# Optimization experiments

Measured on AMD Instinct MI355X. Metric: run time of the kernel, lower is better.

The kernel has to match this reference:

```python
import jax, jax.numpy as jnp
import numpy as np

N = 100000   # nodes per graph
E = 1200000  # edges per graph
D_IN = 64
FILTERS = [128, 128, 64]
K_SLICES = 16
MLP = [32, 16, 8, 4]


def setup_inputs() -> dict:
    key = jax.random.key(0)
    ks = jax.random.split(key, 24)
    s = 0.1
    inp = {
        'x_i': jax.random.normal(ks[0], (N, D_IN), jnp.float32),
        'edge_index_i': jax.random.randint(ks[1], (2, E), 0, N, jnp.int64),
        'x_j': jax.random.normal(ks[2], (N, D_IN), jnp.float32),
        'edge_index_j': jax.random.randint(ks[3], (2, E), 0, N, jnp.int64),
    }
    # GCN conv stack params: 64->128->128->64
    dims = [D_IN] + FILTERS
    for li in range(3):
        inp[f'conv_w{li}'] = jax.random.normal(ks[4 + 2 * li], (dims[li], dims[li + 1]), jnp.float32) * s
        inp[f'conv_b{li}'] = jnp.zeros((dims[li + 1],), jnp.float32)
    d = FILTERS[-1]
    inp['att_w'] = jax.random.normal(ks[10], (d, d), jnp.float32) * s
    inp['ntn_wt'] = jax.random.normal(ks[11], (K_SLICES, d, d), jnp.float32) * s
    inp['ntn_wm'] = jax.random.normal(ks[12], (K_SLICES, 2 * d), jnp.float32) * s
    inp['ntn_b'] = jnp.zeros((K_SLICES,), jnp.float32)
    mdims = [K_SLICES] + MLP
    for li in range(4):
        inp[f'mlp_w{li}'] = jax.random.normal(ks[13 + 2 * li], (mdims[li], mdims[li + 1]), jnp.float32) * s
        inp[f'mlp_b{li}'] = jnp.zeros((mdims[li + 1],), jnp.float32)
    inp['score_w'] = jax.random.normal(ks[22], (MLP[-1], 1), jnp.float32) * s
    inp['score_b'] = jnp.zeros((1,), jnp.float32)
    return inp


def _gcn(x, W, b, src, dst):
    # PyG GCNConv: add self loops, symmetric normalization, aggregate into dst.
    n = x.shape[0]
    loop = jnp.arange(n, dtype=src.dtype)
    src = jnp.concatenate([src, loop])
    dst = jnp.concatenate([dst, loop])
    deg = jax.ops.segment_sum(jnp.ones_like(dst, dtype=x.dtype), dst, num_segments=n)
    dinv = jax.lax.rsqrt(deg)  # deg >= 1 due to self loops
    norm = dinv[src] * dinv[dst]             # [E+N]
    xw = x @ W                               # [N, Dout]
    out = jax.ops.segment_sum(xw[src] * norm[:, None], dst, num_segments=n)
    return out + b


def _attention(x, Wa):
    # global context attention pooling over nodes
    gc = jnp.tanh(jnp.mean(x @ Wa, axis=0))          # [D]
    att = jax.nn.sigmoid(x @ gc)                     # [N]
    return jnp.sum(x * att[:, None], axis=0)         # [D]


def _ntn(h_i, h_j, Wt, Wm, b):
    # s_k = h_i^T Wt[k] h_j + Wm[k] . [h_i; h_j] + b_k, then tanh
    bilinear = jnp.einsum('d,kde,e->k', h_i, Wt, h_j)
    linear = Wm @ jnp.concatenate([h_i, h_j])
    return jnp.tanh(bilinear + linear + b)           # [K]


def reference(x_i, edge_index_i, x_j, edge_index_j,
              conv_w0, conv_b0, conv_w1, conv_b1, conv_w2, conv_b2,
              att_w, ntn_wt, ntn_wm, ntn_b,
              mlp_w0, mlp_b0, mlp_w1, mlp_b1, mlp_w2, mlp_b2, mlp_w3, mlp_b3,
              score_w, score_b):
    convs = [(conv_w0, conv_b0), (conv_w1, conv_b1), (conv_w2, conv_b2)]
    si, di = edge_index_i[0], edge_index_i[1]
    sj, dj = edge_index_j[0], edge_index_j[1]
    for li, (W, b) in enumerate(convs):
        x_i = _gcn(x_i, W, b, si, di)
        x_j = _gcn(x_j, W, b, sj, dj)
        if li < len(convs) - 1:
            x_i = jax.nn.relu(x_i)
            x_j = jax.nn.relu(x_j)
    h_i = _attention(x_i, att_w)
    h_j = _attention(x_j, att_w)
    z = _ntn(h_i, h_j, ntn_wt, ntn_wm, ntn_b)        # [K]
    for W, b in [(mlp_w0, mlp_b0), (mlp_w1, mlp_b1), (mlp_w2, mlp_b2), (mlp_w3, mlp_b3)]:
        z = jax.nn.relu(z @ W + b)
    return z @ score_w + score_b                     # [1]
```

## Files before the change

### kernel.cpp

```cpp
#include <hip/hip_runtime.h>
#include <cstdint>
#include <cstddef>

#define CDIV(a,b) (((a)+(b)-1)/(b))

typedef __attribute__((ext_vector_type(8))) unsigned short ushort8v;
typedef __attribute__((ext_vector_type(8))) short short8v;
typedef __attribute__((ext_vector_type(4))) float f32x4;
typedef __attribute__((ext_vector_type(2))) float f32x2;

constexpr int BCAP = 8192;
constexpr int CPAD = 256 * BCAP;

__device__ __forceinline__ float bf2f(unsigned short u) {
  return __uint_as_float(((unsigned)u) << 16);
}
__device__ __forceinline__ unsigned short f2bf(float f) {
  unsigned u = __float_as_uint(f);
  unsigned r = (u + 0x7fff + ((u >> 16) & 1)) >> 16;
  return (unsigned short)r;
}

__device__ __forceinline__ void acc_fp8(float* acc, uint2 v) {
  f32x2 p;
  p = __builtin_amdgcn_cvt_pk_f32_fp8((int)v.x, false); acc[0] += p[0]; acc[1] += p[1];
  p = __builtin_amdgcn_cvt_pk_f32_fp8((int)v.x, true);  acc[2] += p[0]; acc[3] += p[1];
  p = __builtin_amdgcn_cvt_pk_f32_fp8((int)v.y, false); acc[4] += p[0]; acc[5] += p[1];
  p = __builtin_amdgcn_cvt_pk_f32_fp8((int)v.y, true);  acc[6] += p[0]; acc[7] += p[1];
}


__global__ void k_prep(const float* __restrict__ w0, const float* __restrict__ w1,
                       const float* __restrict__ w2,
                       unsigned short* __restrict__ w0p, unsigned short* __restrict__ w1p,
                       unsigned short* __restrict__ w2p,
                       int* __restrict__ gcur, double* __restrict__ gcsum,
                       double* __restrict__ hsum) {
  int id = blockIdx.x * 256 + threadIdx.x;
  if (id < 512) gcur[id] = 0;
  else if (id < 640) gcsum[id - 512] = 0.0;
  else if (id < 768) hsum[id - 640] = 0.0;
  if (id < 8192) {
    int k = id / 128, n = id % 128;
    w0p[n * 64 + ((((k >> 3) + n) & 7) * 8) + (k & 7)] = f2bf(w0[id]);
  }
  if (id < 16384) {
    int k = id / 128, n = id % 128;
    w1p[n * 128 + ((((k >> 3) + n) & 15) * 8) + (k & 7)] = f2bf(w1[id]);
  }
  if (id < 8192) {
    int k = id / 64, n = id % 64;
    w2p[n * 128 + ((((k >> 3) + n) & 15) * 8) + (k & 7)] = f2bf(w2[id]);
  }
}


__global__ __launch_bounds__(256) void k_place(const int* __restrict__ src0,
                                               const int* __restrict__ dst0,
                                               const int* __restrict__ src1,
                                               const int* __restrict__ dst1,
                                               int E, int N,
                                               int* __restrict__ gcur,
                                               unsigned* __restrict__ part) {
  __shared__ int bcnt[256], bbase[256], bcur[256];
  int g = blockIdx.y;
  const int* src = g ? src1 : src0;
  const int* dst = g ? dst1 : dst0;
  int t = threadIdx.x;
  int e0 = blockIdx.x * 4096, e1 = min(e0 + 4096, E);
  bcnt[t] = 0;
  __syncthreads();
  for (int e = e0 + t; e < e1; e += 256) atomicAdd(&bcnt[dst[e] >> 9], 1);
  __syncthreads();
  bbase[t] = t * BCAP + (bcnt[t] ? atomicAdd(&gcur[g * 256 + t], bcnt[t]) : 0);
  bcur[t] = 0;
  __syncthreads();
  unsigned* pg = part + (size_t)g * CPAD;
  for (int e = e0 + t; e < e1; e += 256) {
    int d = dst[e], s = src[e];
    int b = d >> 9;
    int off = atomicAdd(&bcur[b], 1);
    pg[bbase[b] + off] = ((unsigned)(d & 511) << 18) | (unsigned)(s + g * N);
  }
}


__global__ __launch_bounds__(256) void k_build(const unsigned* __restrict__ part,
                                               const int* __restrict__ gcur,
                                               int2* __restrict__ rowp2, int* __restrict__ col,
                                               float* __restrict__ dinv, int n) {
  __shared__ int cnt[512], off[512], tmp[256];
  int g = blockIdx.y, b = blockIdx.x;
  int lo = b << 9;
  if (lo >= n) return;
  int t = threadIdx.x;
  int s0 = b * BCAP;
  int cntE = gcur[g * 256 + b];
  const unsigned* pg = part + (size_t)g * CPAD;
  cnt[t] = 0; cnt[t + 256] = 0;
  __syncthreads();
  for (int e = s0 + t; e < s0 + cntE; e += 256) atomicAdd(&cnt[pg[e] >> 18], 1);
  __syncthreads();
  int a0 = cnt[2 * t], a1 = cnt[2 * t + 1];
  int ps = a0 + a1;
  tmp[t] = ps; __syncthreads();
  for (int o = 1; o < 256; o <<= 1) {
    int x = (t >= o) ? tmp[t - o] : 0;
    __syncthreads();
    tmp[t] += x;
    __syncthreads();
  }
  int ex = tmp[t] - ps;
  off[2 * t] = ex;
  off[2 * t + 1] = ex + a0;
  __syncthreads();
  for (int i = t; i < 512; i += 256) {
    int node = lo + i;
    if (node < n) {
      int st = g * CPAD + s0 + off[i];
      rowp2[g * n + node] = make_int2(st, st + cnt[i]);
      dinv[g * n + node] = rsqrtf((float)(cnt[i] + 1));
    }
  }
  __syncthreads();
  for (int e = s0 + t; e < s0 + cntE; e += 256) {
    unsigned pr = pg[e];
    int p = atomicAdd(&off[pr >> 18], 1);
    col[g * CPAD + s0 + p] = (int)(pr & 0x3FFFFu);
  }
}


__global__ void k_tofp8(const float* __restrict__ in0, const float* __restrict__ in1,
                        const float* __restrict__ dinv,
                        uint2* __restrict__ out, int n8half, int n8) {
  int i = blockIdx.x * blockDim.x + threadIdx.x;
  if (i < n8) {
    const float4* i4 = (i < n8half) ? (const float4*)in0 : (const float4*)in1;
    int ii = (i < n8half) ? i : i - n8half;
    float di = dinv[i >> 3];
    float4 a = i4[2 * ii], b = i4[2 * ii + 1];
    int lo = __builtin_amdgcn_cvt_pk_fp8_f32(di * a.x, di * a.y, 0, false);
    lo = __builtin_amdgcn_cvt_pk_fp8_f32(di * a.z, di * a.w, lo, true);
    int hi = __builtin_amdgcn_cvt_pk_fp8_f32(di * b.x, di * b.y, 0, false);
    hi = __builtin_amdgcn_cvt_pk_fp8_f32(di * b.z, di * b.w, hi, true);
    out[i] = make_uint2((unsigned)lo, (unsigned)hi);
  }
}


template<int D, bool ADD_BIAS, bool COLSUM>
__device__ __forceinline__ void agg_body(
    const unsigned char* __restrict__ xin, unsigned short* __restrict__ xout,
    const int2* __restrict__ rowp2, const int* __restrict__ col,
    const float* __restrict__ dinv, const float* __restrict__ bias, int n,
    float* __restrict__ partial) {
  constexpr int G = D / 8;
  constexpr int NPB = 256 / G;
  int node = blockIdx.x * NPB + threadIdx.x / G;
  int g = threadIdx.x % G;
  const uint2* x8 = (const uint2*)xin;
  float r[8];
  if (node < n) {
    float di = dinv[node];
    float acc[8];
#pragma unroll
    for (int j = 0; j < 8; ++j) acc[j] = 0.f;
    acc_fp8(acc, x8[(size_t)node * G + g]);
    int2 rp = rowp2[node];
    int e = rp.x, e1 = rp.y;
    for (; e + 4 <= e1; e += 4) {
      int s0 = col[e], s1 = col[e + 1], s2 = col[e + 2], s3 = col[e + 3];
      uint2 v0 = x8[(size_t)s0 * G + g];
      uint2 v1 = x8[(size_t)s1 * G + g];
      uint2 v2 = x8[(size_t)s2 * G + g];
      uint2 v3 = x8[(size_t)s3 * G + g];
      acc_fp8(acc, v0); acc_fp8(acc, v1);
      acc_fp8(acc, v2); acc_fp8(acc, v3);
    }
    for (; e < e1; ++e) {
      int s = col[e];
      acc_fp8(acc, x8[(size_t)s * G + g]);
    }
#pragma unroll
    for (int j = 0; j < 8; ++j) {
      r[j] = di * acc[j];
      if (ADD_BIAS) r[j] += bias[g * 8 + j];
    }
    ushort8v o;
#pragma unroll
    for (int j = 0; j < 8; ++j) o[j] = f2bf(r[j]);
    ((ushort8v*)xout)[(size_t)node * G + g] = o;
  } else {
#pragma unroll
    for (int j = 0; j < 8; ++j) r[j] = 0.f;
  }
  if (COLSUM) {
    __shared__ float ws[4][64];
    int lane = threadIdx.x & 63, wave = threadIdx.x >> 6;
#pragma unroll
    for (int j = 0; j < 8; ++j) {
      float v = r[j];
      v += __shfl_xor(v, 8);
      v += __shfl_xor(v, 16);
      v += __shfl_xor(v, 32);
      r[j] = v;
    }
    if (lane < 8) {
#pragma unroll
      for (int j = 0; j < 8; ++j) ws[wave][lane * 8 + j] = r[j];
    }
    __syncthreads();
    int t = threadIdx.x;
    if (t < 64) partial[(size_t)blockIdx.x * 64 + t] = ws[0][t] + ws[1][t] + ws[2][t] + ws[3][t];
  }
}

__global__ __launch_bounds__(256) void k_aggL0(
    const unsigned char* __restrict__ x, unsigned short* __restrict__ o,
    const int2* __restrict__ rp, const int* __restrict__ col,
    const float* __restrict__ dv, int n) {
  agg_body<64, false, false>(x, o, rp, col, dv, nullptr, n, nullptr);
}
__global__ __launch_bounds__(256) void k_aggL1(
    const unsigned char* __restrict__ x, unsigned short* __restrict__ o,
    const int2* __restrict__ rp, const int* __restrict__ col,
    const float* __restrict__ dv, int n) {
  agg_body<128, false, false>(x, o, rp, col, dv, nullptr, n, nullptr);
}
__global__ __launch_bounds__(256) void k_aggF(
    const unsigned char* __restrict__ x, unsigned short* __restrict__ o,
    const int2* __restrict__ rp, const int* __restrict__ col,
    const float* __restrict__ dv, const float* __restrict__ bias, int n,
    float* __restrict__ partial) {
  agg_body<64, true, true>(x, o, rp, col, dv, bias, n, partial);
}


template<int K, int DOUT, bool RELU, bool PRESCALE, bool OUTFP8>
__device__ __forceinline__ void gemm_body(
    const unsigned short* __restrict__ A, const unsigned short* __restrict__ Wp,
    const float* __restrict__ bias, void* __restrict__ Cv,
    const float* __restrict__ dinv, int n) {
  constexpr int CPR = K / 8;
  constexpr int CM = CPR - 1;
  constexpr int NT = DOUT / 16;
  __shared__ unsigned short As[128 * K];
  __shared__ unsigned short Ws[DOUT * K];
  int t = threadIdx.x;
  int blockM = blockIdx.x * 128;

#pragma unroll
  for (int id = t; id < 128 * CPR; id += 256) {
    int r = id / CPR, c = id % CPR;
    int grow = blockM + r;
    ushort8v v = {0, 0, 0, 0, 0, 0, 0, 0};
    if (grow < n) v = ((const ushort8v*)A)[(size_t)grow * CPR + c];
    *(ushort8v*)&As[r * K + ((c + r) & CM) * 8] = v;
  }
#pragma unroll
  for (int id = t; id < DOUT * CPR; id += 256)
    ((ushort8v*)Ws)[id] = ((const ushort8v*)Wp)[id];
  __syncthreads();

  int lane = t & 63, wave = t >> 6;
  int m15 = lane & 15, quad = lane >> 4;
  f32x4 acc[2][NT];
#pragma unroll
  for (int i = 0; i < 2; ++i)
#pragma unroll
    for (int j = 0; j < NT; ++j) acc[i][j] = (f32x4){0.f, 0.f, 0.f, 0.f};

  int i0 = wave * 32 + m15;
  int i1 = i0 + 16;
#pragma unroll
  for (int kc = 0; kc < K; kc += 32) {
    int c0 = (kc >> 3) + quad;
    short8v a0 = *(const short8v*)&As[i0 * K + ((c0 + i0) & CM) * 8];
    short8v a1 = *(const short8v*)&As[i1 * K + ((c0 + i1) & CM) * 8];
    short8v b[NT];
#pragma unroll
    for (int nt = 0; nt < NT; ++nt) {
      int nn = nt * 16 + m15;
      b[nt] = *(const short8v*)&Ws[nn * K + ((c0 + nn) & CM) * 8];
    }
#pragma unroll
    for (int nt = 0; nt < NT; ++nt) {
      acc[0][nt] = __builtin_amdgcn_mfma_f32_16x16x32_bf16(a0, b[nt], acc[0][nt], 0, 0, 0);
      acc[1][nt] = __builtin_amdgcn_mfma_f32_16x16x32_bf16(a1, b[nt], acc[1][nt], 0, 0, 0);
    }
  }

#pragma unroll
  for (int rt = 0; rt < 2; ++rt) {
    int rbase = blockM + wave * 32 + rt * 16 + quad * 4;
#pragma unroll
    for (int nt = 0; nt < NT; ++nt) {
      int colg = nt * 16 + m15;
      float bv = bias ? bias[colg] : 0.f;
#pragma unroll
      for (int r = 0; r < 4; ++r) {
        int row = rbase + r;
        if (row < n) {
          float v = acc[rt][nt][r] + bv;
          if (RELU) v = fmaxf(v, 0.f);
          if (PRESCALE) v *= dinv[row];
          if (OUTFP8) {
            int b8 = __builtin_amdgcn_cvt_pk_fp8_f32(v, v, 0, false);
            ((unsigned char*)Cv)[(size_t)row * DOUT + colg] = (unsigned char)(b8 & 0xff);
          } else {
            ((unsigned short*)Cv)[(size_t)row * DOUT + colg] = f2bf(v);
          }
        }
      }
    }
  }
}

__global__ __launch_bounds__(256) void k_gemmL0(
    const unsigned short* __restrict__ A, const unsigned short* __restrict__ Wp,
    const float* __restrict__ bias, void* __restrict__ C,
    const float* __restrict__ dv, int n) {
  gemm_body<64, 128, true, true, true>(A, Wp, bias, C, dv, n);
}
__global__ __launch_bounds__(256) void k_gemmL1(
    const unsigned short* __restrict__ A, const unsigned short* __restrict__ Wp,
    const float* __restrict__ bias, void* __restrict__ C,
    const float* __restrict__ dv, int n) {
  gemm_body<128, 128, true, false, false>(A, Wp, bias, C, dv, n);
}
__global__ __launch_bounds__(256) void k_gemmL2(
    const unsigned short* __restrict__ A, const unsigned short* __restrict__ Wp,
    const float* __restrict__ bias, void* __restrict__ C,
    const float* __restrict__ dv, int n) {
  gemm_body<128, 64, false, true, true>(A, Wp, bias, C, dv, n);
}


__global__ __launch_bounds__(256) void k_cm2(const float* __restrict__ partial, int nbg,
                                             double* __restrict__ gcsum) {
  __shared__ double sd[256];
  int g = blockIdx.y, t = threadIdx.x;
  int f = t & 63, rg = t >> 6;
  double acc = 0.0;
  for (int b = blockIdx.x * 4 + rg; b < nbg; b += gridDim.x * 4)
    acc += (double)partial[(size_t)(g * nbg + b) * 64 + f];
  sd[t] = acc; __syncthreads();
  if (t < 64) {
    double tot = sd[t] + sd[t + 64] + sd[t + 128] + sd[t + 192];
    atomicAdd(&gcsum[g * 64 + t], tot);
  }
}


__global__ void k_hsum(const unsigned short* __restrict__ x, const double* __restrict__ gcsum,
                       const float* __restrict__ Wa, int N, int n2,
                       double* __restrict__ hsum) {
  __shared__ float m[128], gcs[128];
  __shared__ double sd[256][4];
  int t = threadIdx.x;
  if (t < 128) m[t] = (float)(gcsum[t] / (double)N);
  __syncthreads();
  if (t < 128) {
    int gg = t >> 6, f = t & 63;
    float s = 0.f;
    for (int d = 0; d < 64; ++d) s += m[gg * 64 + d] * Wa[d * 64 + f];
    gcs[t] = tanhf(s);
  }
  __syncthreads();
  int g = t & 15, sub = t >> 4;
  float4 gcv0 = ((const float4*)gcs)[g];
  float4 gcv1 = ((const float4*)gcs)[16 + g];
  double a[2][4];
#pragma unroll
  for (int j = 0; j < 4; ++j) { a[0][j] = 0.0; a[1][j] = 0.0; }
  for (int node = blockIdx.x * 16 + sub; node < n2; node += gridDim.x * 16) {
    int gid = node >= N;
    float4 gcv = gid ? gcv1 : gcv0;
    ushort4 xu = ((const ushort4*)x)[(size_t)node * 16 + g];
    float x0 = bf2f(xu.x), x1 = bf2f(xu.y), x2 = bf2f(xu.z), x3 = bf2f(xu.w);
    float p = x0 * gcv.x + x1 * gcv.y + x2 * gcv.z + x3 * gcv.w;
    p += __shfl_xor(p, 1);
    p += __shfl_xor(p, 2);
    p += __shfl_xor(p, 4);
    p += __shfl_xor(p, 8);
    float att = 1.f / (1.f + expf(-p));
    a[gid][0] += (double)(att * x0); a[gid][1] += (double)(att * x1);
    a[gid][2] += (double)(att * x2); a[gid][3] += (double)(att * x3);
  }
#pragma unroll 1
  for (int gid = 0; gid < 2; ++gid) {
    sd[t][0] = a[gid][0]; sd[t][1] = a[gid][1];
    sd[t][2] = a[gid][2]; sd[t][3] = a[gid][3];
    __syncthreads();
    if (t < 64) {
      int gg = t >> 2, j = t & 3;
      double tot = 0;
      for (int w = 0; w < 16; ++w) tot += sd[w * 16 + gg][j];
      if (tot != 0.0) atomicAdd(&hsum[gid * 64 + t], tot);
    }
    __syncthreads();
  }
}


__global__ __launch_bounds__(1024) void k_final(
    const double* __restrict__ hsum,
    const float* __restrict__ Wt, const float* __restrict__ Wm,
    const float* __restrict__ bn,
    const float* __restrict__ w0, const float* __restrict__ b0,
    const float* __restrict__ w1, const float* __restrict__ b1,
    const float* __restrict__ w2, const float* __restrict__ b2,
    const float* __restrict__ w3, const float* __restrict__ b3,
    const float* __restrict__ sw, const float* __restrict__ sb,
    float* __restrict__ out) {
  __shared__ float hi[64], hj[64], red[1024], z[16], u[32], v[16], w[8], q[4];
  int t = threadIdx.x;
  if (t < 64) hi[t] = (float)hsum[t];
  else if (t < 128) hj[t - 64] = (float)hsum[t];
  __syncthreads();
  int k = t >> 6, r = t & 63;
  const float* wr = Wt + ((size_t)k * 64 + r) * 64;
  float s = 0.f;
#pragma unroll 8
  for (int c = 0; c < 64; ++c) s += wr[c] * hj[c];
  float p = hi[r] * s;
  p += Wm[k * 128 + r] * hi[r] + Wm[k * 128 + 64 + r] * hj[r];
  red[t] = p;
  __syncthreads();
  for (int o = 32; o > 0; o >>= 1) {
    if (r < o) red[t] += red[t + o];
    __syncthreads();
  }
  if (t < 16) z[t] = tanhf(red[t * 64] + bn[t]);
  __syncthreads();
  if (t < 32) {
    float ss = b0[t];
    for (int i = 0; i < 16; ++i) ss += z[i] * w0[i * 32 + t];
    u[t] = fmaxf(ss, 0.f);
  }
  __syncthreads();
  if (t < 16) {
    float ss = b1[t];
    for (int i = 0; i < 32; ++i) ss += u[i] * w1[i * 16 + t];
    v[t] = fmaxf(ss, 0.f);
  }
  __syncthreads();
  if (t < 8) {
    float ss = b2[t];
    for (int i = 0; i < 16; ++i) ss += v[i] * w2[i * 8 + t];
    w[t] = fmaxf(ss, 0.f);
  }
  __syncthreads();
  if (t < 4) {
    float ss = b3[t];
    for (int i = 0; i < 8; ++i) ss += w[i] * w3[i * 4 + t];
    q[t] = fmaxf(ss, 0.f);
  }
  __syncthreads();
  if (t == 0) {
    float ss = sb[0];
    for (int i = 0; i < 4; ++i) ss += q[i] * sw[i];
    out[0] = ss;
  }
}


extern "C" void kernel_launch(void* const* d_in, const int* in_sizes, int n_in,
                              void* d_out, int out_size, void* d_ws, size_t ws_size,
                              hipStream_t stream) {
  const float* x_i = (const float*)d_in[0];
  const int*   ei  = (const int*)d_in[1];
  const float* x_j = (const float*)d_in[2];
  const int*   ej  = (const int*)d_in[3];
  const float* cw0 = (const float*)d_in[4];  const float* cb0 = (const float*)d_in[5];
  const float* cw1 = (const float*)d_in[6];  const float* cb1 = (const float*)d_in[7];
  const float* cw2 = (const float*)d_in[8];  const float* cb2 = (const float*)d_in[9];
  const float* aw  = (const float*)d_in[10];
  const float* wt  = (const float*)d_in[11]; const float* wm  = (const float*)d_in[12];
  const float* bn  = (const float*)d_in[13];
  const float* m0w = (const float*)d_in[14]; const float* m0b = (const float*)d_in[15];
  const float* m1w = (const float*)d_in[16]; const float* m1b = (const float*)d_in[17];
  const float* m2w = (const float*)d_in[18]; const float* m2b = (const float*)d_in[19];
  const float* m3w = (const float*)d_in[20]; const float* m3b = (const float*)d_in[21];
  const float* sw  = (const float*)d_in[22]; const float* sb  = (const float*)d_in[23];

  int N = in_sizes[0] / 64;
  int E = in_sizes[1] / 2;
  int N2 = 2 * N;

  char* p = (char*)d_ws;
  auto alloc = [&](size_t b) -> void* {
    void* r = (void*)p;
    p += (b + 255) & ~(size_t)255;
    return r;
  };
  int*    gcur    = (int*)alloc(512 * 4);
  double* gcsum   = (double*)alloc(128 * 8);
  double* hsum    = (double*)alloc(128 * 8);
  int2*   rowp2   = (int2*)alloc((size_t)N2 * 8);
  int*    col     = (int*)alloc((size_t)2 * CPAD * 4);
  float*  dinv    = (float*)alloc((size_t)N2 * 4);
  float*  partial = (float*)alloc((size_t)CDIV(N2, 32) * 64 * 4);
  unsigned short* w0p = (unsigned short*)alloc(64 * 128 * 2);
  unsigned short* w1p = (unsigned short*)alloc(128 * 128 * 2);
  unsigned short* w2p = (unsigned short*)alloc(128 * 64 * 2);
  char* S1 = (char*)alloc((size_t)N2 * 128 * 2);
  char* S2 = (char*)alloc((size_t)N2 * 128 * 2);

  k_prep<<<64, 256, 0, stream>>>(cw0, cw1, cw2, w0p, w1p, w2p, gcur, gcsum, hsum);

  unsigned* part = (unsigned*)S1;
  k_place<<<dim3(CDIV(E, 4096), 2), 256, 0, stream>>>(ei, ei + E, ej, ej + E, E, N, gcur, part);
  k_build<<<dim3(256, 2), 256, 0, stream>>>(part, gcur, rowp2, col, dinv, N);

  unsigned char* xf8 = (unsigned char*)S2;
  k_tofp8<<<CDIV(N2 * 8, 256), 256, 0, stream>>>(x_i, x_j, dinv, (uint2*)xf8, N * 8, N2 * 8);

  unsigned short* A0 = (unsigned short*)S1;
  unsigned char*  G0 = (unsigned char*)S2;
  unsigned short* A1 = (unsigned short*)S1;
  unsigned short* G1 = (unsigned short*)S2;
  unsigned char*  G2 = (unsigned char*)S1;
  unsigned short* F  = (unsigned short*)S2;

  k_aggL0<<<CDIV(N2, 32), 256, 0, stream>>>(xf8, A0, rowp2, col, dinv, N2);
  k_gemmL0<<<CDIV(N2, 128), 256, 0, stream>>>(A0, w0p, cb0, G0, dinv, N2);
  k_aggL1<<<CDIV(N2, 16), 256, 0, stream>>>(G0, A1, rowp2, col, dinv, N2);
  k_gemmL1<<<CDIV(N2, 128), 256, 0, stream>>>(A1, w1p, cb1, G1, dinv, N2);
  k_gemmL2<<<CDIV(N2, 128), 256, 0, stream>>>(G1, w2p, nullptr, G2, dinv, N2);
  k_aggF<<<CDIV(N2, 32), 256, 0, stream>>>(G2, F, rowp2, col, dinv, cb2, N2, partial);

  k_cm2<<<dim3(32, 2), 256, 0, stream>>>(partial, N / 32, gcsum);
  k_hsum<<<1024, 256, 0, stream>>>(F, gcsum, aw, N, N2, hsum);

  k_final<<<1, 1024, 0, stream>>>(hsum, wt, wm, bn,
                                  m0w, m0b, m1w, m1b, m2w, m2b, m3w, m3b,
                                  sw, sb, (float*)d_out);
}
```

Before: 509.1 us.

## Load GEMM operands directly from global memory, dropping LDS staging

The dense GEMM no longer stages the A tile and the packed weights through shared memory with a swizzled layout. Each lane now loads its bf16 MFMA fragments straight from global memory, and the weights are repacked unswizzled in row-major n×k order. This removes the LDS write/read traffic, the barrier and the LDS footprint, which may allow higher occupancy. In exchange, every wave rereads the weight matrix from global/L2 for each row tile, and the A loads become strided 16-byte gathers.

New measurement: 535.5 us. 5.2% more time.

```diff
diff --git a/kernel.cpp b/kernel.cpp
--- a/kernel.cpp
+++ b/kernel.cpp
@@ -42,15 +42,15 @@
   else if (id < 768) hsum[id - 640] = 0.0;
   if (id < 8192) {
     int k = id / 128, n = id % 128;
-    w0p[n * 64 + ((((k >> 3) + n) & 7) * 8) + (k & 7)] = f2bf(w0[id]);
+    w0p[n * 64 + k] = f2bf(w0[id]);
   }
   if (id < 16384) {
     int k = id / 128, n = id % 128;
-    w1p[n * 128 + ((((k >> 3) + n) & 15) * 8) + (k & 7)] = f2bf(w1[id]);
+    w1p[n * 128 + k] = f2bf(w1[id]);
   }
   if (id < 8192) {
     int k = id / 64, n = id % 64;
-    w2p[n * 128 + ((((k >> 3) + n) & 15) * 8) + (k & 7)] = f2bf(w2[id]);
+    w2p[n * 128 + k] = f2bf(w2[id]);
   }
 }
 
@@ -242,52 +242,31 @@
     const unsigned short* __restrict__ A, const unsigned short* __restrict__ Wp,
     const float* __restrict__ bias, void* __restrict__ Cv,
     const float* __restrict__ dinv, int n) {
-  constexpr int CPR = K / 8;
-  constexpr int CM = CPR - 1;
   constexpr int NT = DOUT / 16;
-  __shared__ unsigned short As[128 * K];
-  __shared__ unsigned short Ws[DOUT * K];
   int t = threadIdx.x;
-  int blockM = blockIdx.x * 128;
-
-#pragma unroll
-  for (int id = t; id < 128 * CPR; id += 256) {
-    int r = id / CPR, c = id % CPR;
-    int grow = blockM + r;
-    ushort8v v = {0, 0, 0, 0, 0, 0, 0, 0};
-    if (grow < n) v = ((const ushort8v*)A)[(size_t)grow * CPR + c];
-    *(ushort8v*)&As[r * K + ((c + r) & CM) * 8] = v;
-  }
-#pragma unroll
-  for (int id = t; id < DOUT * CPR; id += 256)
-    ((ushort8v*)Ws)[id] = ((const ushort8v*)Wp)[id];
-  __syncthreads();
-
   int lane = t & 63, wave = t >> 6;
   int m15 = lane & 15, quad = lane >> 4;
+  int blockM = blockIdx.x * 128;
+  int i0 = blockM + wave * 32 + m15;
+  int i1 = i0 + 16;
+  int i0c = min(i0, n - 1), i1c = min(i1, n - 1);
+
   f32x4 acc[2][NT];
 #pragma unroll
   for (int i = 0; i < 2; ++i)
 #pragma unroll
     for (int j = 0; j < NT; ++j) acc[i][j] = (f32x4){0.f, 0.f, 0.f, 0.f};
 
-  int i0 = wave * 32 + m15;
-  int i1 = i0 + 16;
 #pragma unroll
   for (int kc = 0; kc < K; kc += 32) {
-    int c0 = (kc >> 3) + quad;
-    short8v a0 = *(const short8v*)&As[i0 * K + ((c0 + i0) & CM) * 8];
-    short8v a1 = *(const short8v*)&As[i1 * K + ((c0 + i1) & CM) * 8];
-    short8v b[NT];
+    int ko = kc + quad * 8;
+    short8v a0 = *(const short8v*)&A[(size_t)i0c * K + ko];
+    short8v a1 = *(const short8v*)&A[(size_t)i1c * K + ko];
 #pragma unroll
     for (int nt = 0; nt < NT; ++nt) {
-      int nn = nt * 16 + m15;
-      b[nt] = *(const short8v*)&Ws[nn * K + ((c0 + nn) & CM) * 8];
-    }
-#pragma unroll
-    for (int nt = 0; nt < NT; ++nt) {
-      acc[0][nt] = __builtin_amdgcn_mfma_f32_16x16x32_bf16(a0, b[nt], acc[0][nt], 0, 0, 0);
-      acc[1][nt] = __builtin_amdgcn_mfma_f32_16x16x32_bf16(a1, b[nt], acc[1][nt], 0, 0, 0);
+      short8v b = *(const short8v*)&Wp[(size_t)(nt * 16 + m15) * K + ko];
+      acc[0][nt] = __builtin_amdgcn_mfma_f32_16x16x32_bf16(a0, b, acc[0][nt], 0, 0, 0);
+      acc[1][nt] = __builtin_amdgcn_mfma_f32_16x16x32_bf16(a1, b, acc[1][nt], 0, 0, 0);
     }
   }
 
```
